# Kernel optimization log

Measured on AMD Instinct MI355X. Metric: run time of the kernel, lower is better.

The kernel has to match this reference:

```python
import jax, jax.numpy as jnp
import numpy as np
import math

N_NODES = 100000
N_EDGES = 1600000
IN_FEATS = 64
H_FEATS = 64
NUM_CLASSES = 2
LS_D = [2, 4, 6, 8]
LS_COEFF = [1.0, 1.0, 1.0, 1.0]
K = 4  # polynomial order per conv (len of each theta)


def _chi_theta(d, coeff):
    # Faithful port of calculate_theta_Chi for d > 0: fit chi-square-like
    # density on [0,2] with a degree-3 Chebyshev series, reverse coeffs.
    n = 2 * d
    m = 1.0 / (n / 2 + 1)  # i = n/2 - 1, m = 1/(i+2)
    def y(x):
        x = np.asarray(x, dtype=np.float64)
        return 1.0 / (2 ** (n / 2) * math.gamma(n / 2)) * (x / m) ** (n / 2 - 1) * np.exp(-(x / m) / 2)
    xs = np.linspace(0.0, 2.0, 20001)
    S = np.trapz(y(xs), xs)  # dense trapezoid ~ scipy.integrate.quad on [0,2]
    lambs = np.linspace(0.0, 2.0, 500)
    c = np.polynomial.chebyshev.chebfit(lambs, y(lambs) / S, 3)
    return (c[::-1] * coeff).astype(np.float32)

THETAS_NP = np.stack([_chi_theta(d, c) for d, c in zip(LS_D, LS_COEFF)])  # [4, K]


def setup_inputs() -> dict:
    key = jax.random.key(0)
    ks = jax.random.split(key, 8)
    sc = 0.05
    return {
        "x": jax.random.normal(ks[0], (N_NODES, IN_FEATS), dtype=jnp.float32),
        "src": jax.random.randint(ks[1], (N_EDGES,), 0, N_NODES, dtype=jnp.int32),
        "dst": jax.random.randint(ks[2], (N_EDGES,), 0, N_NODES, dtype=jnp.int32),
        "thetas": jnp.asarray(THETAS_NP),
        "W1": jax.random.normal(ks[3], (IN_FEATS, H_FEATS), dtype=jnp.float32) * sc,
        "b1": jnp.zeros((H_FEATS,), dtype=jnp.float32),
        "W2": jax.random.normal(ks[4], (H_FEATS, H_FEATS), dtype=jnp.float32) * sc,
        "b2": jnp.zeros((H_FEATS,), dtype=jnp.float32),
        "Wm1": jax.random.normal(ks[5], (H_FEATS * len(LS_D), H_FEATS), dtype=jnp.float32) * sc,
        "bm1": jnp.zeros((H_FEATS,), dtype=jnp.float32),
        "Wm2": jax.random.normal(ks[6], (H_FEATS, NUM_CLASSES), dtype=jnp.float32) * sc,
        "bm2": jnp.zeros((NUM_CLASSES,), dtype=jnp.float32),
    }


def reference(x, src, dst, thetas, W1, b1, W2, b2, Wm1, bm1, Wm2, bm2):
    n = x.shape[0]
    # input MLP stem
    h = jax.nn.relu(x @ W1 + b1)
    h = jax.nn.relu(h @ W2 + b2)
    # D^{-1/2} from in-degrees (clamped to >= 1), as in DGL in_degrees()
    deg = jax.ops.segment_sum(jnp.ones_like(dst, dtype=h.dtype), dst, num_segments=n)
    dinv = jnp.maximum(deg, 1.0) ** -0.5  # [N]
    dinv = dinv[:, None]  # [N, 1]
    # shared Laplacian power sequence: feats[k] = L^k h with L = I - D^-1/2 A D^-1/2
    feats = [h]
    f = h
    for _ in range(K - 1):
        t = f * dinv                                   # [N, H]
        agg = jax.ops.segment_sum(t[src], dst, num_segments=n)  # gather-scatter SpMM
        f = f - agg * dinv
        feats.append(f)
    F = jnp.stack(feats)  # [K, N, H]
    # per-conv polynomial combination, then concat along feature dim
    h_final = jnp.einsum('ck,knh->nch', thetas, F).reshape(n, -1)  # [N, C*H]
    # output MLP (2 layers)
    h_out = jax.nn.relu(h_final @ Wm1 + bm1)
    return h_out @ Wm2 + bm2
```

## Files before the change

kernel.cpp:

```cpp
#include <hip/hip_runtime.h>
#include <math.h>

#define FSTRIDE 256
#define BCAP2 4608
#define CHUNK 8192

__device__ __forceinline__ void fma4(float4& a, float s, const float4& b) {
    a.x = fmaf(s, b.x, a.x);
    a.y = fmaf(s, b.y, a.y);
    a.z = fmaf(s, b.z, a.z);
    a.w = fmaf(s, b.w, a.w);
}

__device__ __forceinline__ unsigned short f2bf(float f) {
    unsigned int u = __builtin_bit_cast(unsigned int, f);
    u += 0x7fff + ((u >> 16) & 1);
    return (unsigned short)(u >> 16);
}
__device__ __forceinline__ float bf2f(unsigned short s) {
    return __builtin_bit_cast(float, ((unsigned int)s) << 16);
}

__global__ void zero_k(int* __restrict__ p, int n) {
    int i = blockIdx.x * blockDim.x + threadIdx.x;
    int st = gridDim.x * blockDim.x;
    for (; i < n; i += st) p[i] = 0;
}

__global__ __launch_bounds__(256) void part1_k(const int* __restrict__ src,
        const int* __restrict__ dst, int* __restrict__ gcnt,
        unsigned int* __restrict__ pairs, int E, int NB) {
    __shared__ int lcnt[512];
    __shared__ int lbase[512];
    __shared__ int lpos[512];
    int tid = threadIdx.x;
    int base = blockIdx.x * CHUNK;
    int m = E - base; if (m > CHUNK) m = CHUNK;
    for (int b = tid; b < NB; b += 256) { lcnt[b] = 0; lpos[b] = 0; }
    __syncthreads();
    for (int i = tid; i < m; i += 256)
        atomicAdd(&lcnt[dst[base + i] >> 8], 1);
    __syncthreads();
    for (int b = tid; b < NB; b += 256)
        lbase[b] = (lcnt[b] > 0) ? atomicAdd(&gcnt[b], lcnt[b]) : 0;
    __syncthreads();
    for (int i = tid; i < m; i += 256) {
        int s = src[base + i], d = dst[base + i];
        int b = d >> 8;
        int p = atomicAdd(&lpos[b], 1);
        int idx = lbase[b] + p;
        if (idx < BCAP2)
            pairs[(size_t)b * BCAP2 + idx] = (unsigned int)s | ((unsigned int)(d & 255) << 17);
    }
}

__global__ __launch_bounds__(512) void bscan_k(const int* __restrict__ gcnt,
        int* __restrict__ bbase, int* __restrict__ rowp, int NB, int E, int n) {
    __shared__ int buf[512];
    int tid = threadIdx.x;
    int v = (tid < NB) ? (gcnt[tid] > BCAP2 ? BCAP2 : gcnt[tid]) : 0;
    buf[tid] = v;
    __syncthreads();
    int x = v;
    for (int off = 1; off < 512; off <<= 1) {
        int t = (tid >= off) ? buf[tid - off] : 0;
        __syncthreads();
        x += t;
        buf[tid] = x;
        __syncthreads();
    }
    if (tid < NB) bbase[tid] = x - v;
    if (tid == 0) rowp[n] = E;
}

__global__ __launch_bounds__(256) void csr2_k(const int* __restrict__ gcnt,
        const unsigned int* __restrict__ pairs, const int* __restrict__ bbase,
        int* __restrict__ rowp, int* __restrict__ colb, float* __restrict__ dinv, int n) {
    int b = blockIdx.x;
    int tid = threadIdx.x;
    int cntb = gcnt[b]; if (cntb > BCAP2) cntb = BCAP2;
    const unsigned int* pb = pairs + (size_t)b * BCAP2;
    __shared__ int c[256];
    __shared__ int sc[256];
    __shared__ int lpos[256];
    c[tid] = 0; lpos[tid] = 0;
    __syncthreads();
    for (int i = tid; i < cntb; i += 256)
        atomicAdd(&c[pb[i] >> 17], 1);
    __syncthreads();
    int v = c[tid];
    sc[tid] = v;
    __syncthreads();
    int x = v;
    for (int off = 1; off < 256; off <<= 1) {
        int t = (tid >= off) ? sc[tid - off] : 0;
        __syncthreads();
        x += t;
        sc[tid] = x;
        __syncthreads();
    }
    int ex = x - v;
    sc[tid] = ex;
    int node = b * 256 + tid;
    if (node < n) {
        rowp[node] = bbase[b] + ex;
        dinv[node] = 1.0f / sqrtf((float)(v > 1 ? v : 1));
    }
    __syncthreads();
    for (int i = tid; i < cntb; i += 256) {
        unsigned int pk = pb[i];
        int j = pk >> 17;
        int p = atomicAdd(&lpos[j], 1);
        colb[bbase[b] + sc[j] + p] = (int)(pk & 0x1FFFF);
    }
}

__global__ __launch_bounds__(256) void mlp_k(const float* __restrict__ x,
        const float* __restrict__ W1, const float* __restrict__ b1,
        const float* __restrict__ W2, const float* __restrict__ b2,
        const float* __restrict__ dinv,
        float* __restrict__ F, unsigned short* __restrict__ T0, int n, int ntiles) {
    __shared__ float Ws1[64 * 64];
    __shared__ float Ws2[64 * 64];
    __shared__ float xT[64 * 68];
    int tid = threadIdx.x;
    int ti = tid >> 4, tj = tid & 15;
    for (int idx = tid; idx < 4096; idx += 256) { Ws1[idx] = W1[idx]; Ws2[idx] = W2[idx]; }
    float4 b1v = *(const float4*)&b1[4 * tj];
    float4 b2v = *(const float4*)&b2[4 * tj];

    for (int g = blockIdx.x; g < ntiles; g += gridDim.x) {
        int base = g * 64;
        __syncthreads();
        for (int it = 0; it < 4; it++) {
            int node = ti + it * 16;
            int gn = base + node;
            float4 v = make_float4(0.f, 0.f, 0.f, 0.f);
            if (gn < n) v = *(const float4*)&x[(size_t)gn * 64 + 4 * tj];
            xT[(4 * tj + 0) * 68 + node] = v.x;
            xT[(4 * tj + 1) * 68 + node] = v.y;
            xT[(4 * tj + 2) * 68 + node] = v.z;
            xT[(4 * tj + 3) * 68 + node] = v.w;
        }
        __syncthreads();

        float4 a0 = b1v, a1 = b1v, a2 = b1v, a3 = b1v;
        #pragma unroll 8
        for (int k = 0; k < 64; k++) {
            float4 xv = *(const float4*)&xT[k * 68 + 4 * ti];
            float4 wv = *(const float4*)&Ws1[k * 64 + 4 * tj];
            fma4(a0, xv.x, wv); fma4(a1, xv.y, wv); fma4(a2, xv.z, wv); fma4(a3, xv.w, wv);
        }
        __syncthreads();
        {
            int hb = (4 * tj) * 68 + 4 * ti;
            xT[hb + 0 * 68 + 0] = fmaxf(a0.x, 0.f);
            xT[hb + 1 * 68 + 0] = fmaxf(a0.y, 0.f);
            xT[hb + 2 * 68 + 0] = fmaxf(a0.z, 0.f);
            xT[hb + 3 * 68 + 0] = fmaxf(a0.w, 0.f);
            xT[hb + 0 * 68 + 1] = fmaxf(a1.x, 0.f);
            xT[hb + 1 * 68 + 1] = fmaxf(a1.y, 0.f);
            xT[hb + 2 * 68 + 1] = fmaxf(a1.z, 0.f);
            xT[hb + 3 * 68 + 1] = fmaxf(a1.w, 0.f);
            xT[hb + 0 * 68 + 2] = fmaxf(a2.x, 0.f);
            xT[hb + 1 * 68 + 2] = fmaxf(a2.y, 0.f);
            xT[hb + 2 * 68 + 2] = fmaxf(a2.z, 0.f);
            xT[hb + 3 * 68 + 2] = fmaxf(a2.w, 0.f);
            xT[hb + 0 * 68 + 3] = fmaxf(a3.x, 0.f);
            xT[hb + 1 * 68 + 3] = fmaxf(a3.y, 0.f);
            xT[hb + 2 * 68 + 3] = fmaxf(a3.z, 0.f);
            xT[hb + 3 * 68 + 3] = fmaxf(a3.w, 0.f);
        }
        __syncthreads();

        a0 = b2v; a1 = b2v; a2 = b2v; a3 = b2v;
        #pragma unroll 8
        for (int k = 0; k < 64; k++) {
            float4 xv = *(const float4*)&xT[k * 68 + 4 * ti];
            float4 wv = *(const float4*)&Ws2[k * 64 + 4 * tj];
            fma4(a0, xv.x, wv); fma4(a1, xv.y, wv); fma4(a2, xv.z, wv); fma4(a3, xv.w, wv);
        }
        int gn0 = base + 4 * ti;
#define STORE_ROW(ai, ii)                                                                  \
        {                                                                                  \
            int gn = gn0 + (ii);                                                           \
            if (gn < n) {                                                                  \
                float r0 = fmaxf(ai.x, 0.f), r1 = fmaxf(ai.y, 0.f);                        \
                float r2 = fmaxf(ai.z, 0.f), r3 = fmaxf(ai.w, 0.f);                        \
                *(float4*)&F[(size_t)gn * FSTRIDE + 4 * tj] = make_float4(r0, r1, r2, r3); \
                float dg = dinv[gn];                                                       \
                ushort4 tv;                                                                \
                tv.x = f2bf(r0 * dg); tv.y = f2bf(r1 * dg);                                \
                tv.z = f2bf(r2 * dg); tv.w = f2bf(r3 * dg);                                \
                *(ushort4*)&T0[(size_t)gn * 64 + 4 * tj] = tv;                             \
            }                                                                              \
        }
        STORE_ROW(a0, 0) STORE_ROW(a1, 1) STORE_ROW(a2, 2) STORE_ROW(a3, 3)
#undef STORE_ROW
    }
}

__global__ void wm1p_k(const float* __restrict__ thetas, const float* __restrict__ Wm1,
                       float* __restrict__ Wm1p) {
    int idx = blockIdx.x * blockDim.x + threadIdx.x;
    if (idx >= 16384) return;
    int j = idx & 63;
    int q = idx >> 6;
    int k = q >> 6;
    int hh = q & 63;
    float a = 0.f;
    for (int c = 0; c < 4; c++) a += thetas[c * 4 + k] * Wm1[(c * 64 + hh) * 64 + j];
    Wm1p[idx] = a;
}

__global__ __launch_bounds__(256) void prop_k(const float* __restrict__ Fin,
        float* __restrict__ Fout,
        const unsigned short* __restrict__ Tin, unsigned short* __restrict__ Tout,
        const int* __restrict__ rowp, const int* __restrict__ colb,
        const float* __restrict__ dinv, int n, int writeT) {
    int gw = (blockIdx.x * blockDim.x + threadIdx.x) >> 6;
    int lane = threadIdx.x & 63;
    if (gw >= n) return;
    int beg = rowp[gw], end = rowp[gw + 1];
    float a0 = 0.f, a1 = 0.f, a2 = 0.f, a3 = 0.f;
    int e = beg;
    for (; e + 7 < end; e += 8) {
        int s0 = colb[e],     s1 = colb[e + 1], s2 = colb[e + 2], s3 = colb[e + 3];
        int s4 = colb[e + 4], s5 = colb[e + 5], s6 = colb[e + 6], s7 = colb[e + 7];
        float f0 = bf2f(Tin[(size_t)s0 * 64 + lane]);
        float f1 = bf2f(Tin[(size_t)s1 * 64 + lane]);
        float f2 = bf2f(Tin[(size_t)s2 * 64 + lane]);
        float f3 = bf2f(Tin[(size_t)s3 * 64 + lane]);
        float f4 = bf2f(Tin[(size_t)s4 * 64 + lane]);
        float f5 = bf2f(Tin[(size_t)s5 * 64 + lane]);
        float f6 = bf2f(Tin[(size_t)s6 * 64 + lane]);
        float f7 = bf2f(Tin[(size_t)s7 * 64 + lane]);
        a0 += f0; a1 += f1; a2 += f2; a3 += f3;
        a0 += f4; a1 += f5; a2 += f6; a3 += f7;
    }
    for (; e + 3 < end; e += 4) {
        int s0 = colb[e], s1 = colb[e + 1], s2 = colb[e + 2], s3 = colb[e + 3];
        a0 += bf2f(Tin[(size_t)s0 * 64 + lane]);
        a1 += bf2f(Tin[(size_t)s1 * 64 + lane]);
        a2 += bf2f(Tin[(size_t)s2 * 64 + lane]);
        a3 += bf2f(Tin[(size_t)s3 * 64 + lane]);
    }
    for (; e < end; ++e)
        a0 += bf2f(Tin[(size_t)colb[e] * 64 + lane]);
    float acc = (a0 + a1) + (a2 + a3);
    float dg = dinv[gw];
    float fo = Fin[(size_t)gw * FSTRIDE + lane] - acc * dg;
    Fout[(size_t)gw * FSTRIDE + lane] = fo;
    if (writeT) Tout[(size_t)gw * 64 + lane] = f2bf(fo * dg);
}

__global__ __launch_bounds__(512, 4) void final_k(const float* __restrict__ F,
        const float* __restrict__ Wm1p, const float* __restrict__ bm1,
        const float* __restrict__ Wm2, const float* __restrict__ bm2,
        float* __restrict__ out, int n, int ntiles) {
    __shared__ float Ws[256 * 64];
    int tid = threadIdx.x;
    int ti = tid >> 4, tj = tid & 15;
    for (int idx = tid; idx < 16384; idx += 512) Ws[idx] = Wm1p[idx];
    float4 bv = *(const float4*)&bm1[4 * tj];
    float2 w2a = ((const float2*)Wm2)[4 * tj + 0];
    float2 w2b = ((const float2*)Wm2)[4 * tj + 1];
    float2 w2c = ((const float2*)Wm2)[4 * tj + 2];
    float2 w2d = ((const float2*)Wm2)[4 * tj + 3];
    float bo0 = bm2[0], bo1 = bm2[1];
    __syncthreads();

    for (int g = blockIdx.x; g < ntiles; g += gridDim.x) {
        int base = g * 128;
        const float* fr = &F[(size_t)(base + 4 * ti) * FSTRIDE];
        float4 a0 = bv, a1 = bv, a2 = bv, a3 = bv;
        #pragma unroll 8
        for (int k = 0; k < 256; k += 4) {
            float4 w0 = *(const float4*)&Ws[(k + 0) * 64 + 4 * tj];
            float4 w1 = *(const float4*)&Ws[(k + 1) * 64 + 4 * tj];
            float4 w2 = *(const float4*)&Ws[(k + 2) * 64 + 4 * tj];
            float4 w3 = *(const float4*)&Ws[(k + 3) * 64 + 4 * tj];
            float4 r;
            r = *(const float4*)&fr[k];
            fma4(a0, r.x, w0); fma4(a0, r.y, w1); fma4(a0, r.z, w2); fma4(a0, r.w, w3);
            r = *(const float4*)&fr[FSTRIDE + k];
            fma4(a1, r.x, w0); fma4(a1, r.y, w1); fma4(a1, r.z, w2); fma4(a1, r.w, w3);
            r = *(const float4*)&fr[2 * FSTRIDE + k];
            fma4(a2, r.x, w0); fma4(a2, r.y, w1); fma4(a2, r.z, w2); fma4(a2, r.w, w3);
            r = *(const float4*)&fr[3 * FSTRIDE + k];
            fma4(a3, r.x, w0); fma4(a3, r.y, w1); fma4(a3, r.z, w2); fma4(a3, r.w, w3);
        }
#define EMIT(ai, ii)                                                             \
        {                                                                        \
            float o0 = fmaxf(ai.x,0.f)*w2a.x + fmaxf(ai.y,0.f)*w2b.x             \
                     + fmaxf(ai.z,0.f)*w2c.x + fmaxf(ai.w,0.f)*w2d.x;            \
            float o1 = fmaxf(ai.x,0.f)*w2a.y + fmaxf(ai.y,0.f)*w2b.y             \
                     + fmaxf(ai.z,0.f)*w2c.y + fmaxf(ai.w,0.f)*w2d.y;            \
            o0 += __shfl_xor(o0, 1); o1 += __shfl_xor(o1, 1);                    \
            o0 += __shfl_xor(o0, 2); o1 += __shfl_xor(o1, 2);                    \
            o0 += __shfl_xor(o0, 4); o1 += __shfl_xor(o1, 4);                    \
            o0 += __shfl_xor(o0, 8); o1 += __shfl_xor(o1, 8);                    \
            int node = base + 4 * ti + (ii);                                     \
            if (tj == 0 && node < n) { out[node * 2] = o0 + bo0;                 \
                                       out[node * 2 + 1] = o1 + bo1; }           \
        }
        EMIT(a0, 0) EMIT(a1, 1) EMIT(a2, 2) EMIT(a3, 3)
#undef EMIT
    }
}

extern "C" void kernel_launch(void* const* d_in, const int* in_sizes, int n_in,
                              void* d_out, int out_size, void* d_ws, size_t ws_size,
                              hipStream_t stream) {
    const float* x      = (const float*)d_in[0];
    const int*   src    = (const int*)d_in[1];
    const int*   dst    = (const int*)d_in[2];
    const float* thetas = (const float*)d_in[3];
    const float* W1     = (const float*)d_in[4];
    const float* b1     = (const float*)d_in[5];
    const float* W2     = (const float*)d_in[6];
    const float* b2     = (const float*)d_in[7];
    const float* Wm1    = (const float*)d_in[8];
    const float* bm1    = (const float*)d_in[9];
    const float* Wm2    = (const float*)d_in[10];
    const float* bm2    = (const float*)d_in[11];
    float* out = (float*)d_out;

    int n = in_sizes[0] / 64;
    int E = in_sizes[1];
    int ntiles  = (n + 63) / 64;
    int ntiles2 = (n + 127) / 128;
    int nn = ntiles2 * 128;
    int NB = (n + 255) / 256;

    float* Fbuf  = (float*)d_ws;
    float* dinv  = Fbuf + (size_t)nn * FSTRIDE;
    int*   rowp  = (int*)(dinv + n);
    int*   colb  = rowp + (n + 1);
    float* Wm1p  = (float*)(colb + E);
    int*   gcnt  = (int*)(Wm1p + 16384);
    int*   bbase = gcnt + NB;
    size_t uoff = (((size_t)(bbase + NB) - (size_t)d_ws) + 255) & ~(size_t)255;
    unsigned int*   pairs = (unsigned int*)((char*)d_ws + uoff);
    unsigned short* Ta    = (unsigned short*)pairs;
    unsigned short* Tb    = Ta + (size_t)n * 64;

    int nchunksP = (E + CHUNK - 1) / CHUNK;

    zero_k<<<4, 256, 0, stream>>>(gcnt, NB);
    part1_k<<<nchunksP, 256, 0, stream>>>(src, dst, gcnt, pairs, E, NB);
    bscan_k<<<1, 512, 0, stream>>>(gcnt, bbase, rowp, NB, E, n);
    csr2_k<<<NB, 256, 0, stream>>>(gcnt, pairs, bbase, rowp, colb, dinv, n);

    mlp_k<<<768, 256, 0, stream>>>(x, W1, b1, W2, b2, dinv, Fbuf, Ta, n, ntiles);
    wm1p_k<<<64, 256, 0, stream>>>(thetas, Wm1, Wm1p);

    prop_k<<<((size_t)n * 64 + 255) / 256, 256, 0, stream>>>(
        Fbuf + 0 * 64, Fbuf + 1 * 64, Ta, Tb, rowp, colb, dinv, n, 1);
    prop_k<<<((size_t)n * 64 + 255) / 256, 256, 0, stream>>>(
        Fbuf + 1 * 64, Fbuf + 2 * 64, Tb, Ta, rowp, colb, dinv, n, 1);
    prop_k<<<((size_t)n * 64 + 255) / 256, 256, 0, stream>>>(
        Fbuf + 2 * 64, Fbuf + 3 * 64, Ta, Tb, rowp, colb, dinv, n, 0);

    final_k<<<512, 512, 0, stream>>>(Fbuf, Wm1p, bm1, Wm2, bm2, out, n, ntiles2);
}
```

Baseline: 320.1 us.

## Feed final MLP from concatenated bf16 scaled features instead of fp32 F buffer

New measurement: 317.6 us. No clear change (-0.8%).

```diff
diff --git a/kernel.cpp b/kernel.cpp
--- a/kernel.cpp
+++ b/kernel.cpp
@@ -1,9 +1,10 @@
 #include <hip/hip_runtime.h>
 #include <math.h>
 
-#define FSTRIDE 256
+#define FS3 192
+#define TS  256
 #define BCAP2 4608
-#define CHUNK 8192
+#define CHUNK 4096
 
 __device__ __forceinline__ void fma4(float4& a, float s, const float4& b) {
     a.x = fmaf(s, b.x, a.x);
@@ -19,6 +20,12 @@
 }
 __device__ __forceinline__ float bf2f(unsigned short s) {
     return __builtin_bit_cast(float, ((unsigned int)s) << 16);
+}
+__device__ __forceinline__ float bflo(unsigned int u) {
+    return __builtin_bit_cast(float, u << 16);
+}
+__device__ __forceinline__ float bfhi(unsigned int u) {
+    return __builtin_bit_cast(float, u & 0xffff0000u);
 }
 
 __global__ void zero_k(int* __restrict__ p, int n) {
@@ -119,7 +126,7 @@
         const float* __restrict__ W1, const float* __restrict__ b1,
         const float* __restrict__ W2, const float* __restrict__ b2,
         const float* __restrict__ dinv,
-        float* __restrict__ F, unsigned short* __restrict__ T0, int n, int ntiles) {
+        float* __restrict__ F, unsigned short* __restrict__ Tcat, int n, int ntiles) {
     __shared__ float Ws1[64 * 64];
     __shared__ float Ws2[64 * 64];
     __shared__ float xT[64 * 68];
@@ -187,12 +194,12 @@
             if (gn < n) {                                                                  \
                 float r0 = fmaxf(ai.x, 0.f), r1 = fmaxf(ai.y, 0.f);                        \
                 float r2 = fmaxf(ai.z, 0.f), r3 = fmaxf(ai.w, 0.f);                        \
-                *(float4*)&F[(size_t)gn * FSTRIDE + 4 * tj] = make_float4(r0, r1, r2, r3); \
+                *(float4*)&F[(size_t)gn * FS3 + 4 * tj] = make_float4(r0, r1, r2, r3);     \
                 float dg = dinv[gn];                                                       \
                 ushort4 tv;                                                                \
                 tv.x = f2bf(r0 * dg); tv.y = f2bf(r1 * dg);                                \
                 tv.z = f2bf(r2 * dg); tv.w = f2bf(r3 * dg);                                \
-                *(ushort4*)&T0[(size_t)gn * 64 + 4 * tj] = tv;                             \
+                *(ushort4*)&Tcat[(size_t)gn * TS + 4 * tj] = tv;                           \
             }                                                                              \
         }
         STORE_ROW(a0, 0) STORE_ROW(a1, 1) STORE_ROW(a2, 2) STORE_ROW(a3, 3)
@@ -217,7 +224,7 @@
         float* __restrict__ Fout,
         const unsigned short* __restrict__ Tin, unsigned short* __restrict__ Tout,
         const int* __restrict__ rowp, const int* __restrict__ colb,
-        const float* __restrict__ dinv, int n, int writeT) {
+        const float* __restrict__ dinv, int n, int writeF) {
     int gw = (blockIdx.x * blockDim.x + threadIdx.x) >> 6;
     int lane = threadIdx.x & 63;
     if (gw >= n) return;
@@ -227,34 +234,35 @@
     for (; e + 7 < end; e += 8) {
         int s0 = colb[e],     s1 = colb[e + 1], s2 = colb[e + 2], s3 = colb[e + 3];
         int s4 = colb[e + 4], s5 = colb[e + 5], s6 = colb[e + 6], s7 = colb[e + 7];
-        float f0 = bf2f(Tin[(size_t)s0 * 64 + lane]);
-        float f1 = bf2f(Tin[(size_t)s1 * 64 + lane]);
-        float f2 = bf2f(Tin[(size_t)s2 * 64 + lane]);
-        float f3 = bf2f(Tin[(size_t)s3 * 64 + lane]);
-        float f4 = bf2f(Tin[(size_t)s4 * 64 + lane]);
-        float f5 = bf2f(Tin[(size_t)s5 * 64 + lane]);
-        float f6 = bf2f(Tin[(size_t)s6 * 64 + lane]);
-        float f7 = bf2f(Tin[(size_t)s7 * 64 + lane]);
+        float f0 = bf2f(Tin[(size_t)s0 * TS + lane]);
+        float f1 = bf2f(Tin[(size_t)s1 * TS + lane]);
+        float f2 = bf2f(Tin[(size_t)s2 * TS + lane]);
+        float f3 = bf2f(Tin[(size_t)s3 * TS + lane]);
+        float f4 = bf2f(Tin[(size_t)s4 * TS + lane]);
+        float f5 = bf2f(Tin[(size_t)s5 * TS + lane]);
+        float f6 = bf2f(Tin[(size_t)s6 * TS + lane]);
+        float f7 = bf2f(Tin[(size_t)s7 * TS + lane]);
         a0 += f0; a1 += f1; a2 += f2; a3 += f3;
         a0 += f4; a1 += f5; a2 += f6; a3 += f7;
     }
     for (; e + 3 < end; e += 4) {
         int s0 = colb[e], s1 = colb[e + 1], s2 = colb[e + 2], s3 = colb[e + 3];
-        a0 += bf2f(Tin[(size_t)s0 * 64 + lane]);
-        a1 += bf2f(Tin[(size_t)s1 * 64 + lane]);
-        a2 += bf2f(Tin[(size_t)s2 * 64 + lane]);
-        a3 += bf2f(Tin[(size_t)s3 * 64 + lane]);
+        a0 += bf2f(Tin[(size_t)s0 * TS + lane]);
+        a1 += bf2f(Tin[(size_t)s1 * TS + lane]);
+        a2 += bf2f(Tin[(size_t)s2 * TS + lane]);
+        a3 += bf2f(Tin[(size_t)s3 * TS + lane]);
     }
     for (; e < end; ++e)
-        a0 += bf2f(Tin[(size_t)colb[e] * 64 + lane]);
+        a0 += bf2f(Tin[(size_t)colb[e] * TS + lane]);
     float acc = (a0 + a1) + (a2 + a3);
     float dg = dinv[gw];
-    float fo = Fin[(size_t)gw * FSTRIDE + lane] - acc * dg;
-    Fout[(size_t)gw * FSTRIDE + lane] = fo;
-    if (writeT) Tout[(size_t)gw * 64 + lane] = f2bf(fo * dg);
-}
-
-__global__ __launch_bounds__(512, 4) void final_k(const float* __restrict__ F,
+    float fo = Fin[(size_t)gw * FS3 + lane] - acc * dg;
+    if (writeF) Fout[(size_t)gw * FS3 + lane] = fo;
+    Tout[(size_t)gw * TS + lane] = f2bf(fo * dg);
+}
+
+__global__ __launch_bounds__(512, 4) void final_k(const unsigned short* __restrict__ Tcat,
+        const float* __restrict__ dinv,
         const float* __restrict__ Wm1p, const float* __restrict__ bm1,
         const float* __restrict__ Wm2, const float* __restrict__ bm2,
         float* __restrict__ out, int n, int ntiles) {
@@ -272,35 +280,44 @@
 
     for (int g = blockIdx.x; g < ntiles; g += gridDim.x) {
         int base = g * 128;
-        const float* fr = &F[(size_t)(base + 4 * ti) * FSTRIDE];
-        float4 a0 = bv, a1 = bv, a2 = bv, a3 = bv;
-        #pragma unroll 8
-        for (int k = 0; k < 256; k += 4) {
+        const unsigned short* tr = &Tcat[(size_t)(base + 4 * ti) * TS];
+        float4 a0 = make_float4(0.f, 0.f, 0.f, 0.f);
+        float4 a1 = a0, a2 = a0, a3 = a0;
+        #pragma unroll 4
+        for (int k = 0; k < 256; k += 8) {
             float4 w0 = *(const float4*)&Ws[(k + 0) * 64 + 4 * tj];
             float4 w1 = *(const float4*)&Ws[(k + 1) * 64 + 4 * tj];
             float4 w2 = *(const float4*)&Ws[(k + 2) * 64 + 4 * tj];
             float4 w3 = *(const float4*)&Ws[(k + 3) * 64 + 4 * tj];
-            float4 r;
-            r = *(const float4*)&fr[k];
-            fma4(a0, r.x, w0); fma4(a0, r.y, w1); fma4(a0, r.z, w2); fma4(a0, r.w, w3);
-            r = *(const float4*)&fr[FSTRIDE + k];
-            fma4(a1, r.x, w0); fma4(a1, r.y, w1); fma4(a1, r.z, w2); fma4(a1, r.w, w3);
-            r = *(const float4*)&fr[2 * FSTRIDE + k];
-            fma4(a2, r.x, w0); fma4(a2, r.y, w1); fma4(a2, r.z, w2); fma4(a2, r.w, w3);
-            r = *(const float4*)&fr[3 * FSTRIDE + k];
-            fma4(a3, r.x, w0); fma4(a3, r.y, w1); fma4(a3, r.z, w2); fma4(a3, r.w, w3);
+            float4 w4 = *(const float4*)&Ws[(k + 4) * 64 + 4 * tj];
+            float4 w5 = *(const float4*)&Ws[(k + 5) * 64 + 4 * tj];
+            float4 w6 = *(const float4*)&Ws[(k + 6) * 64 + 4 * tj];
+            float4 w7 = *(const float4*)&Ws[(k + 7) * 64 + 4 * tj];
+#define ROW(ai, ii)                                                              \
+            {                                                                    \
+                uint4 u = *(const uint4*)&tr[(size_t)(ii) * TS + k];             \
+                fma4(ai, bflo(u.x), w0); fma4(ai, bfhi(u.x), w1);                \
+                fma4(ai, bflo(u.y), w2); fma4(ai, bfhi(u.y), w3);                \
+                fma4(ai, bflo(u.z), w4); fma4(ai, bfhi(u.z), w5);                \
+                fma4(ai, bflo(u.w), w6); fma4(ai, bfhi(u.w), w7);                \
+            }
+            ROW(a0, 0) ROW(a1, 1) ROW(a2, 2) ROW(a3, 3)
+#undef ROW
         }
 #define EMIT(ai, ii)                                                             \
         {                                                                        \
-            float o0 = fmaxf(ai.x,0.f)*w2a.x + fmaxf(ai.y,0.f)*w2b.x             \
-                     + fmaxf(ai.z,0.f)*w2c.x + fmaxf(ai.w,0.f)*w2d.x;            \
-            float o1 = fmaxf(ai.x,0.f)*w2a.y + fmaxf(ai.y,0.f)*w2b.y             \
-                     + fmaxf(ai.z,0.f)*w2c.y + fmaxf(ai.w,0.f)*w2d.y;            \
+            int node = base + 4 * ti + (ii);                                     \
+            float s = (node < n) ? (1.0f / dinv[node]) : 0.f;                    \
+            float h0 = fmaxf(fmaf(ai.x, s, bv.x), 0.f);                          \
+            float h1 = fmaxf(fmaf(ai.y, s, bv.y), 0.f);                          \
+            float h2 = fmaxf(fmaf(ai.z, s, bv.z), 0.f);                          \
+            float h3 = fmaxf(fmaf(ai.w, s, bv.w), 0.f);                          \
+            float o0 = h0 * w2a.x + h1 * w2b.x + h2 * w2c.x + h3 * w2d.x;        \
+            float o1 = h0 * w2a.y + h1 * w2b.y + h2 * w2c.y + h3 * w2d.y;        \
             o0 += __shfl_xor(o0, 1); o1 += __shfl_xor(o1, 1);                    \
             o0 += __shfl_xor(o0, 2); o1 += __shfl_xor(o1, 2);                    \
             o0 += __shfl_xor(o0, 4); o1 += __shfl_xor(o1, 4);                    \
             o0 += __shfl_xor(o0, 8); o1 += __shfl_xor(o1, 8);                    \
-            int node = base + 4 * ti + (ii);                                     \
             if (tj == 0 && node < n) { out[node * 2] = o0 + bo0;                 \
                                        out[node * 2 + 1] = o1 + bo1; }           \
         }
@@ -330,11 +347,11 @@
     int E = in_sizes[1];
     int ntiles  = (n + 63) / 64;
     int ntiles2 = (n + 127) / 128;
-    int nn = ntiles2 * 128;
+    size_t nn2 = (size_t)ntiles2 * 128;
     int NB = (n + 255) / 256;
 
     float* Fbuf  = (float*)d_ws;
-    float* dinv  = Fbuf + (size_t)nn * FSTRIDE;
+    float* dinv  = Fbuf + (size_t)n * FS3;
     int*   rowp  = (int*)(dinv + n);
     int*   colb  = rowp + (n + 1);
     float* Wm1p  = (float*)(colb + E);
@@ -342,8 +359,7 @@
     int*   bbase = gcnt + NB;
     size_t uoff = (((size_t)(bbase + NB) - (size_t)d_ws) + 255) & ~(size_t)255;
     unsigned int*   pairs = (unsigned int*)((char*)d_ws + uoff);
-    unsigned short* Ta    = (unsigned short*)pairs;
-    unsigned short* Tb    = Ta + (size_t)n * 64;
+    unsigned short* Tcat  = (unsigned short*)pairs;
 
     int nchunksP = (E + CHUNK - 1) / CHUNK;
 
@@ -352,15 +368,15 @@
     bscan_k<<<1, 512, 0, stream>>>(gcnt, bbase, rowp, NB, E, n);
     csr2_k<<<NB, 256, 0, stream>>>(gcnt, pairs, bbase, rowp, colb, dinv, n);
 
-    mlp_k<<<768, 256, 0, stream>>>(x, W1, b1, W2, b2, dinv, Fbuf, Ta, n, ntiles);
+    mlp_k<<<768, 256, 0, stream>>>(x, W1, b1, W2, b2, dinv, Fbuf, Tcat, n, ntiles);
     wm1p_k<<<64, 256, 0, stream>>>(thetas, Wm1, Wm1p);
 
     prop_k<<<((size_t)n * 64 + 255) / 256, 256, 0, stream>>>(
-        Fbuf + 0 * 64, Fbuf + 1 * 64, Ta, Tb, rowp, colb, dinv, n, 1);
+        Fbuf + 0 * 64, Fbuf + 1 * 64, Tcat + 0 * 64, Tcat + 1 * 64, rowp, colb, dinv, n, 1);
     prop_k<<<((size_t)n * 64 + 255) / 256, 256, 0, stream>>>(
-        Fbuf + 1 * 64, Fbuf + 2 * 64, Tb, Ta, rowp, colb, dinv, n, 1);
+        Fbuf + 1 * 64, Fbuf + 2 * 64, Tcat + 1 * 64, Tcat + 2 * 64, rowp, colb, dinv, n, 1);
     prop_k<<<((size_t)n * 64 + 255) / 256, 256, 0, stream>>>(
-        Fbuf + 2 * 64, Fbuf + 3 * 64, Ta, Tb, rowp, colb, dinv, n, 0);
-
-    final_k<<<512, 512, 0, stream>>>(Fbuf, Wm1p, bm1, Wm2, bm2, out, n, ntiles2);
-}
+        Fbuf + 2 * 64, Fbuf + 2 * 64, Tcat + 2 * 64, Tcat + 3 * 64, rowp, colb, dinv, n, 0);
+
+    final_k<<<ntiles2, 512, 0, stream>>>(Tcat, dinv, Wm1p, bm1, Wm2, bm2, out, n, ntiles2);
+}
```
